# Kernel optimization log

Measured on AMD Instinct MI355X. Metric: run time of the kernel, lower is better.

## Reference

```python
import jax, jax.numpy as jnp
import numpy as np

T, H, I, E, K, L, R = 1024, 2048, 1024, 16, 2, 4, 16


def setup_inputs() -> dict:
    key = jax.random.key(0)
    ks = jax.random.split(key, 10)
    hidden_states = jax.random.normal(ks[0], (T, H), jnp.float32)
    topk_ids = jax.random.randint(ks[1], (T, K), 0, E, dtype=jnp.int32)
    topk_weights = jax.random.uniform(ks[2], (T, K), jnp.float32)
    lora_indices = jax.random.randint(ks[3], (T,), 0, L, dtype=jnp.int32)
    lora_ranks = jax.random.randint(ks[4], (L,), 1, R + 1, dtype=jnp.int32)
    scalings = jax.random.uniform(ks[5], (L,), jnp.float32) + 0.5
    w1 = jax.random.normal(ks[6], (E, 2 * I, H), jnp.float32) * 0.02  # fused gate+up
    w2 = jax.random.normal(ks[7], (E, H, I), jnp.float32) * 0.02      # down proj
    lora_a = jax.random.normal(ks[8], (L, E, R, H), jnp.float32) * 0.02
    lora_b = jax.random.normal(ks[9], (L, E, H, R), jnp.float32) * 0.02
    return dict(hidden_states=hidden_states, topk_ids=topk_ids, topk_weights=topk_weights,
                lora_indices=lora_indices, lora_ranks=lora_ranks, scalings=scalings,
                w1=w1, w2=w2, lora_a=lora_a, lora_b=lora_b)


def reference(hidden_states, topk_ids, topk_weights, lora_indices, lora_ranks, scalings,
              w1, w2, lora_a, lora_b):
    x = hidden_states  # [T, H]
    # ---- Base FusedMoE (SiLU-gated), dense over all experts then routed ----
    h1 = jnp.einsum('th,efh->tef', x, w1)                 # [T, E, 2I]
    gate, up = jnp.split(h1, 2, axis=-1)                  # [T, E, I] each
    act = jax.nn.silu(gate) * up                          # [T, E, I]
    expert_out = jnp.einsum('tei,ehi->teh', act, w2)      # [T, E, H]
    route = jnp.zeros((T, E), x.dtype).at[jnp.arange(T)[:, None], topk_ids].add(topk_weights)
    base = jnp.einsum('te,teh->th', route, expert_out)    # [T, H]
    # ---- Per-expert LoRA delta (moe_dispatch + grouped LoRA GEMM) ----
    l_pair = jnp.broadcast_to(lora_indices[:, None], (T, K)).reshape(-1)  # [P], P=T*K
    e_pair = topk_ids.reshape(-1)                                         # [P]
    valid = l_pair >= 0
    l_safe = jnp.maximum(l_pair, 0)
    flat_idx = l_safe * E + e_pair                                        # index into [L*E, ...]
    A = jnp.take(lora_a.reshape(L * E, R, H), flat_idx, axis=0)           # [P, R, H]
    B = jnp.take(lora_b.reshape(L * E, H, R), flat_idx, axis=0)           # [P, H, R]
    xp = jnp.repeat(x, K, axis=0)                                         # [P, H]
    a = jnp.einsum('ph,prh->pr', xp, A)                                   # [P, R]
    ranks = jnp.maximum(lora_ranks, 1)
    rmask = jnp.arange(R)[None, :] < ranks[l_safe][:, None]               # variable rank mask
    a = jnp.where(rmask, a, 0.0) * scalings[l_safe][:, None]
    delta = jnp.einsum('pr,phr->ph', a, B)                                # [P, H]
    delta = jnp.where(valid[:, None], delta, 0.0)
    delta = delta.reshape(T, K, H).sum(axis=1)                            # merge (token,k) pairs
    return base + delta
```

## Files before the change

kernel.cpp:

```cpp
#include <hip/hip_runtime.h>
#include <math.h>

constexpr int T = 1024;
constexpr int H = 2048;
constexpr int I = 1024;
constexpr int E = 16;
constexpr int K = 2;
constexpr int L = 4;
constexpr int R = 16;
constexpr int P = T * K;
constexpr int MT_MAX = 32;
constexpr int G_CVT = T * H / (256 * 8);
constexpr int G1 = MT_MAX * 32;
constexpr int G2 = MT_MAX * 64;

typedef __attribute__((ext_vector_type(8))) short bf16x8;
typedef __attribute__((ext_vector_type(4))) float f32x4;

__device__ inline unsigned short f2bf(float f) {
  unsigned u = __builtin_bit_cast(unsigned, f);
  u = (u + 0x7FFFu + ((u >> 16) & 1u)) >> 16;
  return (unsigned short)u;
}

__device__ inline bf16x8 pack8(f32x4 a, f32x4 b) {
  bf16x8 v;
  v[0] = (short)f2bf(a[0]); v[1] = (short)f2bf(a[1]);
  v[2] = (short)f2bf(a[2]); v[3] = (short)f2bf(a[3]);
  v[4] = (short)f2bf(b[0]); v[5] = (short)f2bf(b[1]);
  v[6] = (short)f2bf(b[2]); v[7] = (short)f2bf(b[3]);
  return v;
}

__device__ inline void st8(unsigned short* s, int r, int c, bf16x8 v) {
  int byte = ((r << 6) + c) * 2;
  byte ^= (r & 7) << 4;
  *reinterpret_cast<bf16x8*>(reinterpret_cast<char*>(s) + byte) = v;
}
__device__ inline bf16x8 ld8(const unsigned short* s, int r, int c) {
  int byte = ((r << 6) + c) * 2;
  byte ^= (r & 7) << 4;
  return *reinterpret_cast<const bf16x8*>(reinterpret_cast<const char*>(s) + byte);
}

__global__ __launch_bounds__(256) void prep_kernel(
    const float* __restrict__ x, unsigned short* __restrict__ xb,
    float* __restrict__ out,
    const int* __restrict__ topk_ids, const float* __restrict__ topk_w,
    int* __restrict__ eoff, int* __restrict__ pair_t,
    float* __restrict__ pair_w, int* __restrict__ pair_e,
    int* __restrict__ tile_e, int* __restrict__ tile_m0, int* __restrict__ ntiles) {
  const int tid = threadIdx.x;
  if (blockIdx.x < G_CVT) {
    const int i = (blockIdx.x * 256 + tid) * 8;
    f32x4 a = *reinterpret_cast<const f32x4*>(x + i);
    f32x4 b = *reinterpret_cast<const f32x4*>(x + i + 4);
    *reinterpret_cast<bf16x8*>(xb + i) = pack8(a, b);
    const f32x4 z = {0.f, 0.f, 0.f, 0.f};
    *reinterpret_cast<f32x4*>(out + i) = z;
    *reinterpret_cast<f32x4*>(out + i + 4) = z;
    return;
  }
  __shared__ int cnt[E];
  __shared__ int off[E + 1];
  __shared__ int cur[E];
  if (tid < E) cnt[tid] = 0;
  __syncthreads();
  for (int p = tid; p < P; p += 256) atomicAdd(&cnt[topk_ids[p]], 1);
  __syncthreads();
  if (tid == 0) {
    off[0] = 0;
    for (int e = 0; e < E; ++e) off[e + 1] = off[e] + cnt[e];
    int nt = 0;
    for (int e = 0; e < E; ++e)
      for (int m0 = 0; m0 < cnt[e]; m0 += 128) {
        tile_e[nt] = e;
        tile_m0[nt] = m0;
        ++nt;
      }
    *ntiles = nt;
  }
  __syncthreads();
  if (tid < E) cur[tid] = off[tid];
  if (tid <= E) eoff[tid] = off[tid];
  __syncthreads();
  for (int p = tid; p < P; p += 256) {
    const int e = topk_ids[p];
    const int pos = atomicAdd(&cur[e], 1);
    pair_t[pos] = p / K;
    pair_w[pos] = topk_w[p];
    pair_e[pos] = e;
  }
}

__global__ __launch_bounds__(256) void gemm1_lora(
    const unsigned short* __restrict__ xb, const float* __restrict__ w1,
    const int* __restrict__ eoff, const int* __restrict__ pair_t,
    const int* __restrict__ tile_e, const int* __restrict__ tile_m0,
    const int* __restrict__ ntiles, unsigned short* __restrict__ act,
    const float* __restrict__ x, const float* __restrict__ lora_a,
    const float* __restrict__ lora_b, const int* __restrict__ lora_idx,
    const int* __restrict__ lora_ranks, const float* __restrict__ scalings,
    const int* __restrict__ pair_e, float* __restrict__ out) {
  __shared__ __align__(16) char smem[24576];
  const int tid = threadIdx.x;

  if (blockIdx.x < (unsigned)G1) {
    const int bid = blockIdx.x;
    const int mt = bid >> 5;
    if (mt >= *ntiles) return;
    const int it = bid & 31;
    const int e = tile_e[mt];
    const int m0 = tile_m0[mt];
    const int beg = eoff[e];
    const int cnt = eoff[e + 1] - beg;
    const int i0 = it * 32;

    unsigned short* sX = (unsigned short*)smem;
    unsigned short* sG = (unsigned short*)(smem + 16384);
    unsigned short* sU = (unsigned short*)(smem + 20480);

    const int xr = tid >> 1, xc = (tid & 1) * 32;
    const int gr = tid >> 3, gc = (tid & 7) * 8;

    const int rm = m0 + xr;
    const int tok = (rm < cnt) ? pair_t[beg + rm] : -1;
    const unsigned short* xrow = xb + (size_t)(tok < 0 ? 0 : tok) * H + xc;
    const float* grow = w1 + ((size_t)e * (2 * I) + i0 + gr) * H + gc;
    const float* urow = grow + (size_t)I * H;

    const int lane = tid & 63, wid = tid >> 6;
    const int wm = wid << 5;
    const int fr = lane & 15, fq = lane >> 4;

    f32x4 ag[2][2], au[2][2];
#pragma unroll
    for (int a = 0; a < 2; ++a)
#pragma unroll
      for (int b = 0; b < 2; ++b) {
        ag[a][b] = {0.f, 0.f, 0.f, 0.f};
        au[a][b] = {0.f, 0.f, 0.f, 0.f};
      }

    bf16x8 rx[4];
    f32x4 rg[2], ru[2];
    const bf16x8 zero8 = {0, 0, 0, 0, 0, 0, 0, 0};

    auto LOAD = [&](int kk) {
      if (tok >= 0) {
#pragma unroll
        for (int s = 0; s < 4; ++s)
          rx[s] = *reinterpret_cast<const bf16x8*>(xrow + kk + s * 8);
      } else {
#pragma unroll
        for (int s = 0; s < 4; ++s) rx[s] = zero8;
      }
#pragma unroll
      for (int s = 0; s < 2; ++s) {
        rg[s] = *reinterpret_cast<const f32x4*>(grow + kk + s * 4);
        ru[s] = *reinterpret_cast<const f32x4*>(urow + kk + s * 4);
      }
    };

    constexpr int NT = H / 64;
    LOAD(0);
    for (int t = 0; t < NT; ++t) {
      const bf16x8 wg = pack8(rg[0], rg[1]);
      const bf16x8 wu = pack8(ru[0], ru[1]);
      __syncthreads();
      st8(sX, xr, xc + 0, rx[0]); st8(sX, xr, xc + 8, rx[1]);
      st8(sX, xr, xc + 16, rx[2]); st8(sX, xr, xc + 24, rx[3]);
      st8(sG, gr, gc, wg);
      st8(sU, gr, gc, wu);
      if (t + 1 < NT) LOAD((t + 1) * 64);
      __syncthreads();
#pragma unroll
      for (int kb = 0; kb < 2; ++kb) {
        const int k8 = (kb << 5) + (fq << 3);
        bf16x8 af[2], gf[2], uf[2];
#pragma unroll
        for (int mi = 0; mi < 2; ++mi) af[mi] = ld8(sX, wm + (mi << 4) + fr, k8);
#pragma unroll
        for (int nj = 0; nj < 2; ++nj) {
          gf[nj] = ld8(sG, (nj << 4) + fr, k8);
          uf[nj] = ld8(sU, (nj << 4) + fr, k8);
        }
#pragma unroll
        for (int mi = 0; mi < 2; ++mi)
#pragma unroll
          for (int nj = 0; nj < 2; ++nj) {
            ag[mi][nj] = __builtin_amdgcn_mfma_f32_16x16x32_bf16(af[mi], gf[nj], ag[mi][nj], 0, 0, 0);
            au[mi][nj] = __builtin_amdgcn_mfma_f32_16x16x32_bf16(af[mi], uf[nj], au[mi][nj], 0, 0, 0);
          }
      }
    }

#pragma unroll
    for (int mi = 0; mi < 2; ++mi)
#pragma unroll
      for (int q = 0; q < 4; ++q) {
        const int m = m0 + wm + (mi << 4) + (fq << 2) + q;
        if (m >= cnt) continue;
#pragma unroll
        for (int nj = 0; nj < 2; ++nj) {
          const float g = ag[mi][nj][q];
          const float u = au[mi][nj][q];
          const float s = g / (1.f + __expf(-g));
          act[(size_t)(beg + m) * I + i0 + (nj << 4) + fr] = f2bf(s * u);
        }
      }
    return;
  }

  const int p = blockIdx.x - G1;
  const int t = pair_t[p];
  const int e = pair_e[p];
  const int l = lora_idx[t];
  if (l < 0) return;
  int rank = lora_ranks[l];
  if (rank < 1) rank = 1;
  const float sc = scalings[l];

  float* a_sh = (float*)smem;
  const int wave = tid >> 6, lane = tid & 63;
  const float4* xv = reinterpret_cast<const float4*>(x + (size_t)t * H);
  const float* Ab = lora_a + (size_t)(l * E + e) * R * H;
#pragma unroll
  for (int q = 0; q < 4; ++q) {
    const int r = (wave << 2) | q;
    const float4* Av = reinterpret_cast<const float4*>(Ab + (size_t)r * H);
    float s = 0.f;
#pragma unroll
    for (int it = 0; it < H / 256; ++it) {
      const int h4 = it * 64 + lane;
      const float4 xx = xv[h4];
      const float4 aa = Av[h4];
      s += xx.x * aa.x + xx.y * aa.y + xx.z * aa.z + xx.w * aa.w;
    }
#pragma unroll
    for (int off = 32; off; off >>= 1) s += __shfl_xor(s, off);
    if (lane == 0) a_sh[r] = (r < rank) ? s * sc : 0.f;
  }
  __syncthreads();
  const float* Bb = lora_b + (size_t)(l * E + e) * H * R;
  for (int h = tid; h < H; h += 256) {
    const float4* Bv = reinterpret_cast<const float4*>(Bb + (size_t)h * R);
    float d = 0.f;
#pragma unroll
    for (int r4 = 0; r4 < 4; ++r4) {
      const float4 bb = Bv[r4];
      d += a_sh[r4 * 4 + 0] * bb.x + a_sh[r4 * 4 + 1] * bb.y +
           a_sh[r4 * 4 + 2] * bb.z + a_sh[r4 * 4 + 3] * bb.w;
    }
    atomicAdd(out + (size_t)t * H + h, d);
  }
}

__global__ __launch_bounds__(256) void gemm2_mfma(
    const unsigned short* __restrict__ act, const float* __restrict__ w2,
    const int* __restrict__ eoff, const int* __restrict__ pair_t,
    const float* __restrict__ pair_w, const int* __restrict__ tile_e,
    const int* __restrict__ tile_m0, const int* __restrict__ ntiles,
    float* __restrict__ out) {
  const int bid = blockIdx.x;
  const int mt = bid >> 6;
  if (mt >= *ntiles) return;
  const int ht = bid & 63;
  const int e = tile_e[mt];
  const int m0 = tile_m0[mt];
  const int beg = eoff[e];
  const int cnt = eoff[e + 1] - beg;
  const int h0 = ht * 32;

  __shared__ unsigned short sA[128 * 64];
  __shared__ unsigned short sB[32 * 64];

  const int tid = threadIdx.x;
  const int ar = tid >> 1, ac = (tid & 1) * 32;
  const int br = tid >> 3, bc = (tid & 7) * 8;

  const bool av = (m0 + ar) < cnt;
  const unsigned short* arow = act + (size_t)(beg + (av ? m0 + ar : 0)) * I + ac;
  const float* brow = w2 + ((size_t)e * H + h0 + br) * I + bc;

  const int lane = tid & 63, wid = tid >> 6;
  const int wm = wid << 5;
  const int fr = lane & 15, fq = lane >> 4;

  f32x4 acc[2][2];
#pragma unroll
  for (int a = 0; a < 2; ++a)
#pragma unroll
    for (int b = 0; b < 2; ++b) acc[a][b] = {0.f, 0.f, 0.f, 0.f};

  bf16x8 ra[4];
  f32x4 rb[2];

  auto LOAD = [&](int kk) {
#pragma unroll
    for (int s = 0; s < 4; ++s)
      ra[s] = *reinterpret_cast<const bf16x8*>(arow + kk + s * 8);
#pragma unroll
    for (int s = 0; s < 2; ++s)
      rb[s] = *reinterpret_cast<const f32x4*>(brow + kk + s * 4);
  };

  constexpr int NT = I / 64;
  LOAD(0);
  for (int t = 0; t < NT; ++t) {
    const bf16x8 wb = pack8(rb[0], rb[1]);
    __syncthreads();
    st8(sA, ar, ac + 0, ra[0]); st8(sA, ar, ac + 8, ra[1]);
    st8(sA, ar, ac + 16, ra[2]); st8(sA, ar, ac + 24, ra[3]);
    st8(sB, br, bc, wb);
    if (t + 1 < NT) LOAD((t + 1) * 64);
    __syncthreads();
#pragma unroll
    for (int kb = 0; kb < 2; ++kb) {
      const int k8 = (kb << 5) + (fq << 3);
      bf16x8 af[2], bf[2];
#pragma unroll
      for (int mi = 0; mi < 2; ++mi) af[mi] = ld8(sA, wm + (mi << 4) + fr, k8);
#pragma unroll
      for (int nj = 0; nj < 2; ++nj) bf[nj] = ld8(sB, (nj << 4) + fr, k8);
#pragma unroll
      for (int mi = 0; mi < 2; ++mi)
#pragma unroll
        for (int nj = 0; nj < 2; ++nj)
          acc[mi][nj] = __builtin_amdgcn_mfma_f32_16x16x32_bf16(af[mi], bf[nj], acc[mi][nj], 0, 0, 0);
    }
  }

#pragma unroll
  for (int mi = 0; mi < 2; ++mi)
#pragma unroll
    for (int q = 0; q < 4; ++q) {
      const int m = m0 + wm + (mi << 4) + (fq << 2) + q;
      if (m >= cnt) continue;
      const int tt = pair_t[beg + m];
      const float w = pair_w[beg + m];
#pragma unroll
      for (int nj = 0; nj < 2; ++nj)
        atomicAdd(out + (size_t)tt * H + h0 + (nj << 4) + fr, w * acc[mi][nj][q]);
    }
}

extern "C" void kernel_launch(void* const* d_in, const int* in_sizes, int n_in,
                              void* d_out, int out_size, void* d_ws, size_t ws_size,
                              hipStream_t stream) {
  const float* x          = (const float*)d_in[0];
  const int*   topk_ids   = (const int*)d_in[1];
  const float* topk_w     = (const float*)d_in[2];
  const int*   lora_idx   = (const int*)d_in[3];
  const int*   lora_ranks = (const int*)d_in[4];
  const float* scalings   = (const float*)d_in[5];
  const float* w1         = (const float*)d_in[6];
  const float* w2         = (const float*)d_in[7];
  const float* lora_a     = (const float*)d_in[8];
  const float* lora_b     = (const float*)d_in[9];
  float* out = (float*)d_out;

  char* ws = (char*)d_ws;
  int*   eoff    = (int*)(ws);
  int*   ntiles  = (int*)(ws + 96);
  int*   tile_e  = (int*)(ws + 256);
  int*   tile_m0 = (int*)(ws + 384);
  int*   pair_t  = (int*)(ws + 512);
  int*   pair_e  = (int*)(ws + 512 + 4 * P);
  float* pair_w  = (float*)(ws + 512 + 8 * P);
  unsigned short* xb  = (unsigned short*)(ws + 32768);
  unsigned short* act = (unsigned short*)(ws + 32768 + (size_t)T * H * 2);

  prep_kernel<<<G_CVT + 1, 256, 0, stream>>>(x, xb, out, topk_ids, topk_w, eoff,
                                             pair_t, pair_w, pair_e, tile_e, tile_m0, ntiles);
  gemm1_lora<<<G1 + P, 256, 0, stream>>>(xb, w1, eoff, pair_t, tile_e, tile_m0, ntiles,
                                         act, x, lora_a, lora_b, lora_idx, lora_ranks,
                                         scalings, pair_e, out);
  gemm2_mfma<<<G2, 256, 0, stream>>>(act, w2, eoff, pair_t, pair_w, tile_e, tile_m0,
                                     ntiles, out);
}
```

Baseline: 177.2 us.

## Merge gemm1, LoRA and gemm2 into one persistent work-queue kernel

Replaces the separate gemm1+LoRA and gemm2 launches with a single persistent kernel of 768 blocks that pulls work items from a global atomic counter. Gemm1 tiles go first, then LoRA pairs, then gemm2 tiles. Each gemm2 tile spins on a per-tile completion counter that its gemm1 tiles increment, so the two GEMM stages can overlap instead of waiting on a full kernel boundary. It also avoids launching empty blocks for nonexistent tiles. The costs are atomic queue traffic, spin-wait stalls, and a dependence on forward progress.

```diff
diff --git a/kernel.cpp b/kernel.cpp
--- a/kernel.cpp
+++ b/kernel.cpp
@@ -9,10 +9,8 @@
 constexpr int L = 4;
 constexpr int R = 16;
 constexpr int P = T * K;
-constexpr int MT_MAX = 32;
 constexpr int G_CVT = T * H / (256 * 8);
-constexpr int G1 = MT_MAX * 32;
-constexpr int G2 = MT_MAX * 64;
+constexpr int GRID = 768;
 
 typedef __attribute__((ext_vector_type(8))) short bf16x8;
 typedef __attribute__((ext_vector_type(4))) float f32x4;
@@ -49,7 +47,8 @@
     const int* __restrict__ topk_ids, const float* __restrict__ topk_w,
     int* __restrict__ eoff, int* __restrict__ pair_t,
     float* __restrict__ pair_w, int* __restrict__ pair_e,
-    int* __restrict__ tile_e, int* __restrict__ tile_m0, int* __restrict__ ntiles) {
+    int* __restrict__ tile_e, int* __restrict__ tile_m0, int* __restrict__ ntiles,
+    int* __restrict__ q, int* __restrict__ done) {
   const int tid = threadIdx.x;
   if (blockIdx.x < G_CVT) {
     const int i = (blockIdx.x * 256 + tid) * 8;
@@ -64,6 +63,8 @@
   __shared__ int cnt[E];
   __shared__ int off[E + 1];
   __shared__ int cur[E];
+  if (tid == 0) *q = 0;
+  if (tid < 32) done[tid] = 0;
   if (tid < E) cnt[tid] = 0;
   __syncthreads();
   for (int p = tid; p < P; p += 256) atomicAdd(&cnt[topk_ids[p]], 1);
@@ -93,256 +94,265 @@
   }
 }
 
-__global__ __launch_bounds__(256) void gemm1_lora(
-    const unsigned short* __restrict__ xb, const float* __restrict__ w1,
-    const int* __restrict__ eoff, const int* __restrict__ pair_t,
-    const int* __restrict__ tile_e, const int* __restrict__ tile_m0,
-    const int* __restrict__ ntiles, unsigned short* __restrict__ act,
-    const float* __restrict__ x, const float* __restrict__ lora_a,
-    const float* __restrict__ lora_b, const int* __restrict__ lora_idx,
-    const int* __restrict__ lora_ranks, const float* __restrict__ scalings,
-    const int* __restrict__ pair_e, float* __restrict__ out) {
+__global__ __launch_bounds__(256, 3) void moe_queue(
+    const unsigned short* xb, const float* w1, const float* w2,
+    const int* eoff, const int* pair_t, const float* pair_w, const int* pair_e,
+    const int* tile_e, const int* tile_m0, const int* ntiles,
+    unsigned short* act,
+    const float* x, const float* lora_a, const float* lora_b,
+    const int* lora_idx, const int* lora_ranks, const float* scalings,
+    float* out, int* q, int* done) {
   __shared__ __align__(16) char smem[24576];
+  __shared__ int sh_item;
   const int tid = threadIdx.x;
-
-  if (blockIdx.x < (unsigned)G1) {
-    const int bid = blockIdx.x;
-    const int mt = bid >> 5;
-    if (mt >= *ntiles) return;
-    const int it = bid & 31;
-    const int e = tile_e[mt];
-    const int m0 = tile_m0[mt];
-    const int beg = eoff[e];
-    const int cnt = eoff[e + 1] - beg;
-    const int i0 = it * 32;
-
-    unsigned short* sX = (unsigned short*)smem;
-    unsigned short* sG = (unsigned short*)(smem + 16384);
-    unsigned short* sU = (unsigned short*)(smem + 20480);
-
-    const int xr = tid >> 1, xc = (tid & 1) * 32;
-    const int gr = tid >> 3, gc = (tid & 7) * 8;
-
-    const int rm = m0 + xr;
-    const int tok = (rm < cnt) ? pair_t[beg + rm] : -1;
-    const unsigned short* xrow = xb + (size_t)(tok < 0 ? 0 : tok) * H + xc;
-    const float* grow = w1 + ((size_t)e * (2 * I) + i0 + gr) * H + gc;
-    const float* urow = grow + (size_t)I * H;
-
-    const int lane = tid & 63, wid = tid >> 6;
-    const int wm = wid << 5;
-    const int fr = lane & 15, fq = lane >> 4;
-
-    f32x4 ag[2][2], au[2][2];
-#pragma unroll
-    for (int a = 0; a < 2; ++a)
-#pragma unroll
-      for (int b = 0; b < 2; ++b) {
-        ag[a][b] = {0.f, 0.f, 0.f, 0.f};
-        au[a][b] = {0.f, 0.f, 0.f, 0.f};
-      }
-
-    bf16x8 rx[4];
-    f32x4 rg[2], ru[2];
-    const bf16x8 zero8 = {0, 0, 0, 0, 0, 0, 0, 0};
-
-    auto LOAD = [&](int kk) {
-      if (tok >= 0) {
+  const int nt = *ntiles;
+  const int n1 = nt * 32;
+  const int n2 = nt * 64;
+  const int total = n1 + P + n2;
+
+  for (;;) {
+    __syncthreads();
+    if (tid == 0) sh_item = atomicAdd(q, 1);
+    __syncthreads();
+    const int item = sh_item;
+    if (item >= total) break;
+
+    if (item < n1) {
+      const int mt = item >> 5;
+      const int it = item & 31;
+      const int e = tile_e[mt];
+      const int m0 = tile_m0[mt];
+      const int beg = eoff[e];
+      const int cnt = eoff[e + 1] - beg;
+      const int i0 = it * 32;
+
+      unsigned short* sX = (unsigned short*)smem;
+      unsigned short* sG = (unsigned short*)(smem + 16384);
+      unsigned short* sU = (unsigned short*)(smem + 20480);
+
+      const int xr = tid >> 1, xc = (tid & 1) * 32;
+      const int gr = tid >> 3, gc = (tid & 7) * 8;
+
+      const int rm = m0 + xr;
+      const int tok = (rm < cnt) ? pair_t[beg + rm] : -1;
+      const unsigned short* xrow = xb + (size_t)(tok < 0 ? 0 : tok) * H + xc;
+      const float* grow = w1 + ((size_t)e * (2 * I) + i0 + gr) * H + gc;
+      const float* urow = grow + (size_t)I * H;
+
+      const int lane = tid & 63, wid = tid >> 6;
+      const int wm = wid << 5;
+      const int fr = lane & 15, fq = lane >> 4;
+
+      f32x4 ag[2][2], au[2][2];
+#pragma unroll
+      for (int a = 0; a < 2; ++a)
+#pragma unroll
+        for (int b = 0; b < 2; ++b) {
+          ag[a][b] = {0.f, 0.f, 0.f, 0.f};
+          au[a][b] = {0.f, 0.f, 0.f, 0.f};
+        }
+
+      bf16x8 rx[4];
+      f32x4 rg[2], ru[2];
+      const bf16x8 zero8 = {0, 0, 0, 0, 0, 0, 0, 0};
+
+      auto LOAD = [&](int kk) {
+        if (tok >= 0) {
+#pragma unroll
+          for (int s = 0; s < 4; ++s)
+            rx[s] = *reinterpret_cast<const bf16x8*>(xrow + kk + s * 8);
+        } else {
+#pragma unroll
+          for (int s = 0; s < 4; ++s) rx[s] = zero8;
+        }
+#pragma unroll
+        for (int s = 0; s < 2; ++s) {
+          rg[s] = *reinterpret_cast<const f32x4*>(grow + kk + s * 4);
+          ru[s] = *reinterpret_cast<const f32x4*>(urow + kk + s * 4);
+        }
+      };
+
+      constexpr int NT = H / 64;
+      LOAD(0);
+      for (int t = 0; t < NT; ++t) {
+        const bf16x8 wg = pack8(rg[0], rg[1]);
+        const bf16x8 wu = pack8(ru[0], ru[1]);
+        __syncthreads();
+        st8(sX, xr, xc + 0, rx[0]); st8(sX, xr, xc + 8, rx[1]);
+        st8(sX, xr, xc + 16, rx[2]); st8(sX, xr, xc + 24, rx[3]);
+        st8(sG, gr, gc, wg);
+        st8(sU, gr, gc, wu);
+        if (t + 1 < NT) LOAD((t + 1) * 64);
+        __syncthreads();
+#pragma unroll
+        for (int kb = 0; kb < 2; ++kb) {
+          const int k8 = (kb << 5) + (fq << 3);
+          bf16x8 af[2], gf[2], uf[2];
+#pragma unroll
+          for (int mi = 0; mi < 2; ++mi) af[mi] = ld8(sX, wm + (mi << 4) + fr, k8);
+#pragma unroll
+          for (int nj = 0; nj < 2; ++nj) {
+            gf[nj] = ld8(sG, (nj << 4) + fr, k8);
+            uf[nj] = ld8(sU, (nj << 4) + fr, k8);
+          }
+#pragma unroll
+          for (int mi = 0; mi < 2; ++mi)
+#pragma unroll
+            for (int nj = 0; nj < 2; ++nj) {
+              ag[mi][nj] = __builtin_amdgcn_mfma_f32_16x16x32_bf16(af[mi], gf[nj], ag[mi][nj], 0, 0, 0);
+              au[mi][nj] = __builtin_amdgcn_mfma_f32_16x16x32_bf16(af[mi], uf[nj], au[mi][nj], 0, 0, 0);
+            }
+        }
+      }
+
+#pragma unroll
+      for (int mi = 0; mi < 2; ++mi)
+#pragma unroll
+        for (int q2 = 0; q2 < 4; ++q2) {
+          const int m = m0 + wm + (mi << 4) + (fq << 2) + q2;
+          if (m >= cnt) continue;
+#pragma unroll
+          for (int nj = 0; nj < 2; ++nj) {
+            const float g = ag[mi][nj][q2];
+            const float u = au[mi][nj][q2];
+            const float s = g / (1.f + __expf(-g));
+            act[(size_t)(beg + m) * I + i0 + (nj << 4) + fr] = f2bf(s * u);
+          }
+        }
+      __syncthreads();
+      if (tid == 0) {
+        __threadfence();
+        atomicAdd(&done[mt], 1);
+      }
+    } else if (item < n1 + P) {
+      const int p = item - n1;
+      const int t = pair_t[p];
+      const int e = pair_e[p];
+      const int l = lora_idx[t];
+      if (l >= 0) {
+        int rank = lora_ranks[l];
+        if (rank < 1) rank = 1;
+        const float sc = scalings[l];
+        float* a_sh = (float*)smem;
+        const int wave = tid >> 6, lane = tid & 63;
+        const float4* xv = reinterpret_cast<const float4*>(x + (size_t)t * H);
+        const float* Ab = lora_a + (size_t)(l * E + e) * R * H;
+#pragma unroll
+        for (int q2 = 0; q2 < 4; ++q2) {
+          const int r = (wave << 2) | q2;
+          const float4* Av = reinterpret_cast<const float4*>(Ab + (size_t)r * H);
+          float s = 0.f;
+#pragma unroll
+          for (int it2 = 0; it2 < H / 256; ++it2) {
+            const int h4 = it2 * 64 + lane;
+            const float4 xx = xv[h4];
+            const float4 aa = Av[h4];
+            s += xx.x * aa.x + xx.y * aa.y + xx.z * aa.z + xx.w * aa.w;
+          }
+#pragma unroll
+          for (int off = 32; off; off >>= 1) s += __shfl_xor(s, off);
+          if (lane == 0) a_sh[r] = (r < rank) ? s * sc : 0.f;
+        }
+        __syncthreads();
+        const float* Bb = lora_b + (size_t)(l * E + e) * H * R;
+        for (int h = tid; h < H; h += 256) {
+          const float4* Bv = reinterpret_cast<const float4*>(Bb + (size_t)h * R);
+          float d = 0.f;
+#pragma unroll
+          for (int r4 = 0; r4 < 4; ++r4) {
+            const float4 bb = Bv[r4];
+            d += a_sh[r4 * 4 + 0] * bb.x + a_sh[r4 * 4 + 1] * bb.y +
+                 a_sh[r4 * 4 + 2] * bb.z + a_sh[r4 * 4 + 3] * bb.w;
+          }
+          atomicAdd(out + (size_t)t * H + h, d);
+        }
+      }
+    } else {
+      const int g = item - n1 - P;
+      const int mt = g >> 6;
+      const int ht = g & 63;
+      while (__hip_atomic_load(&done[mt], __ATOMIC_ACQUIRE, __HIP_MEMORY_SCOPE_AGENT) < 32)
+        __builtin_amdgcn_s_sleep(8);
+      __syncthreads();
+
+      const int e = tile_e[mt];
+      const int m0 = tile_m0[mt];
+      const int beg = eoff[e];
+      const int cnt = eoff[e + 1] - beg;
+      const int h0 = ht * 32;
+
+      unsigned short* sA = (unsigned short*)smem;
+      unsigned short* sB = (unsigned short*)(smem + 16384);
+
+      const int ar = tid >> 1, ac = (tid & 1) * 32;
+      const int br = tid >> 3, bc = (tid & 7) * 8;
+
+      const bool av = (m0 + ar) < cnt;
+      const unsigned short* arow = act + (size_t)(beg + (av ? m0 + ar : 0)) * I + ac;
+      const float* brow = w2 + ((size_t)e * H + h0 + br) * I + bc;
+
+      const int lane = tid & 63, wid = tid >> 6;
+      const int wm = wid << 5;
+      const int fr = lane & 15, fq = lane >> 4;
+
+      f32x4 acc[2][2];
+#pragma unroll
+      for (int a = 0; a < 2; ++a)
+#pragma unroll
+        for (int b = 0; b < 2; ++b) acc[a][b] = {0.f, 0.f, 0.f, 0.f};
+
+      bf16x8 ra[4];
+      f32x4 rb[2];
+
+      auto LOAD = [&](int kk) {
 #pragma unroll
         for (int s = 0; s < 4; ++s)
-          rx[s] = *reinterpret_cast<const bf16x8*>(xrow + kk + s * 8);
-      } else {
-#pragma unroll
-        for (int s = 0; s < 4; ++s) rx[s] = zero8;
-      }
-#pragma unroll
-      for (int s = 0; s < 2; ++s) {
-        rg[s] = *reinterpret_cast<const f32x4*>(grow + kk + s * 4);
-        ru[s] = *reinterpret_cast<const f32x4*>(urow + kk + s * 4);
-      }
-    };
-
-    constexpr int NT = H / 64;
-    LOAD(0);
-    for (int t = 0; t < NT; ++t) {
-      const bf16x8 wg = pack8(rg[0], rg[1]);
-      const bf16x8 wu = pack8(ru[0], ru[1]);
-      __syncthreads();
-      st8(sX, xr, xc + 0, rx[0]); st8(sX, xr, xc + 8, rx[1]);
-      st8(sX, xr, xc + 16, rx[2]); st8(sX, xr, xc + 24, rx[3]);
-      st8(sG, gr, gc, wg);
-      st8(sU, gr, gc, wu);
-      if (t + 1 < NT) LOAD((t + 1) * 64);
-      __syncthreads();
-#pragma unroll
-      for (int kb = 0; kb < 2; ++kb) {
-        const int k8 = (kb << 5) + (fq << 3);
-        bf16x8 af[2], gf[2], uf[2];
-#pragma unroll
-        for (int mi = 0; mi < 2; ++mi) af[mi] = ld8(sX, wm + (mi << 4) + fr, k8);
-#pragma unroll
-        for (int nj = 0; nj < 2; ++nj) {
-          gf[nj] = ld8(sG, (nj << 4) + fr, k8);
-          uf[nj] = ld8(sU, (nj << 4) + fr, k8);
-        }
-#pragma unroll
-        for (int mi = 0; mi < 2; ++mi)
-#pragma unroll
-          for (int nj = 0; nj < 2; ++nj) {
-            ag[mi][nj] = __builtin_amdgcn_mfma_f32_16x16x32_bf16(af[mi], gf[nj], ag[mi][nj], 0, 0, 0);
-            au[mi][nj] = __builtin_amdgcn_mfma_f32_16x16x32_bf16(af[mi], uf[nj], au[mi][nj], 0, 0, 0);
-          }
-      }
-    }
-
-#pragma unroll
-    for (int mi = 0; mi < 2; ++mi)
-#pragma unroll
-      for (int q = 0; q < 4; ++q) {
-        const int m = m0 + wm + (mi << 4) + (fq << 2) + q;
-        if (m >= cnt) continue;
-#pragma unroll
-        for (int nj = 0; nj < 2; ++nj) {
-          const float g = ag[mi][nj][q];
-          const float u = au[mi][nj][q];
-          const float s = g / (1.f + __expf(-g));
-          act[(size_t)(beg + m) * I + i0 + (nj << 4) + fr] = f2bf(s * u);
-        }
-      }
-    return;
-  }
-
-  const int p = blockIdx.x - G1;
-  const int t = pair_t[p];
-  const int e = pair_e[p];
-  const int l = lora_idx[t];
-  if (l < 0) return;
-  int rank = lora_ranks[l];
-  if (rank < 1) rank = 1;
-  const float sc = scalings[l];
-
-  float* a_sh = (float*)smem;
-  const int wave = tid >> 6, lane = tid & 63;
-  const float4* xv = reinterpret_cast<const float4*>(x + (size_t)t * H);
-  const float* Ab = lora_a + (size_t)(l * E + e) * R * H;
-#pragma unroll
-  for (int q = 0; q < 4; ++q) {
-    const int r = (wave << 2) | q;
-    const float4* Av = reinterpret_cast<const float4*>(Ab + (size_t)r * H);
-    float s = 0.f;
-#pragma unroll
-    for (int it = 0; it < H / 256; ++it) {
-      const int h4 = it * 64 + lane;
-      const float4 xx = xv[h4];
-      const float4 aa = Av[h4];
-      s += xx.x * aa.x + xx.y * aa.y + xx.z * aa.z + xx.w * aa.w;
-    }
-#pragma unroll
-    for (int off = 32; off; off >>= 1) s += __shfl_xor(s, off);
-    if (lane == 0) a_sh[r] = (r < rank) ? s * sc : 0.f;
-  }
-  __syncthreads();
-  const float* Bb = lora_b + (size_t)(l * E + e) * H * R;
-  for (int h = tid; h < H; h += 256) {
-    const float4* Bv = reinterpret_cast<const float4*>(Bb + (size_t)h * R);
-    float d = 0.f;
-#pragma unroll
-    for (int r4 = 0; r4 < 4; ++r4) {
-      const float4 bb = Bv[r4];
-      d += a_sh[r4 * 4 + 0] * bb.x + a_sh[r4 * 4 + 1] * bb.y +
-           a_sh[r4 * 4 + 2] * bb.z + a_sh[r4 * 4 + 3] * bb.w;
-    }
-    atomicAdd(out + (size_t)t * H + h, d);
-  }
-}
-
-__global__ __launch_bounds__(256) void gemm2_mfma(
-    const unsigned short* __restrict__ act, const float* __restrict__ w2,
-    const int* __restrict__ eoff, const int* __restrict__ pair_t,
-    const float* __restrict__ pair_w, const int* __restrict__ tile_e,
-    const int* __restrict__ tile_m0, const int* __restrict__ ntiles,
-    float* __restrict__ out) {
-  const int bid = blockIdx.x;
-  const int mt = bid >> 6;
-  if (mt >= *ntiles) return;
-  const int ht = bid & 63;
-  const int e = tile_e[mt];
-  const int m0 = tile_m0[mt];
-  const int beg = eoff[e];
-  const int cnt = eoff[e + 1] - beg;
-  const int h0 = ht * 32;
-
-  __shared__ unsigned short sA[128 * 64];
-  __shared__ unsigned short sB[32 * 64];
-
-  const int tid = threadIdx.x;
-  const int ar = tid >> 1, ac = (tid & 1) * 32;
-  const int br = tid >> 3, bc = (tid & 7) * 8;
-
-  const bool av = (m0 + ar) < cnt;
-  const unsigned short* arow = act + (size_t)(beg + (av ? m0 + ar : 0)) * I + ac;
-  const float* brow = w2 + ((size_t)e * H + h0 + br) * I + bc;
-
-  const int lane = tid & 63, wid = tid >> 6;
-  const int wm = wid << 5;
-  const int fr = lane & 15, fq = lane >> 4;
-
-  f32x4 acc[2][2];
-#pragma unroll
-  for (int a = 0; a < 2; ++a)
-#pragma unroll
-    for (int b = 0; b < 2; ++b) acc[a][b] = {0.f, 0.f, 0.f, 0.f};
-
-  bf16x8 ra[4];
-  f32x4 rb[2];
-
-  auto LOAD = [&](int kk) {
-#pragma unroll
-    for (int s = 0; s < 4; ++s)
-      ra[s] = *reinterpret_cast<const bf16x8*>(arow + kk + s * 8);
-#pragma unroll
-    for (int s = 0; s < 2; ++s)
-      rb[s] = *reinterpret_cast<const f32x4*>(brow + kk + s * 4);
-  };
-
-  constexpr int NT = I / 64;
-  LOAD(0);
-  for (int t = 0; t < NT; ++t) {
-    const bf16x8 wb = pack8(rb[0], rb[1]);
-    __syncthreads();
-    st8(sA, ar, ac + 0, ra[0]); st8(sA, ar, ac + 8, ra[1]);
-    st8(sA, ar, ac + 16, ra[2]); st8(sA, ar, ac + 24, ra[3]);
-    st8(sB, br, bc, wb);
-    if (t + 1 < NT) LOAD((t + 1) * 64);
-    __syncthreads();
-#pragma unroll
-    for (int kb = 0; kb < 2; ++kb) {
-      const int k8 = (kb << 5) + (fq << 3);
-      bf16x8 af[2], bf[2];
-#pragma unroll
-      for (int mi = 0; mi < 2; ++mi) af[mi] = ld8(sA, wm + (mi << 4) + fr, k8);
-#pragma unroll
-      for (int nj = 0; nj < 2; ++nj) bf[nj] = ld8(sB, (nj << 4) + fr, k8);
+          ra[s] = *reinterpret_cast<const bf16x8*>(arow + kk + s * 8);
+#pragma unroll
+        for (int s = 0; s < 2; ++s)
+          rb[s] = *reinterpret_cast<const f32x4*>(brow + kk + s * 4);
+      };
+
+      constexpr int NT2 = I / 64;
+      LOAD(0);
+      for (int t = 0; t < NT2; ++t) {
+        const bf16x8 wb = pack8(rb[0], rb[1]);
+        __syncthreads();
+        st8(sA, ar, ac + 0, ra[0]); st8(sA, ar, ac + 8, ra[1]);
+        st8(sA, ar, ac + 16, ra[2]); st8(sA, ar, ac + 24, ra[3]);
+        st8(sB, br, bc, wb);
+        if (t + 1 < NT2) LOAD((t + 1) * 64);
+        __syncthreads();
+#pragma unroll
+        for (int kb = 0; kb < 2; ++kb) {
+          const int k8 = (kb << 5) + (fq << 3);
+          bf16x8 af[2], bf[2];
+#pragma unroll
+          for (int mi = 0; mi < 2; ++mi) af[mi] = ld8(sA, wm + (mi << 4) + fr, k8);
+#pragma unroll
+          for (int nj = 0; nj < 2; ++nj) bf[nj] = ld8(sB, (nj << 4) + fr, k8);
+#pragma unroll
+          for (int mi = 0; mi < 2; ++mi)
+#pragma unroll
+            for (int nj = 0; nj < 2; ++nj)
+              acc[mi][nj] = __builtin_amdgcn_mfma_f32_16x16x32_bf16(af[mi], bf[nj], acc[mi][nj], 0, 0, 0);
+        }
+      }
+
 #pragma unroll
       for (int mi = 0; mi < 2; ++mi)
 #pragma unroll
-        for (int nj = 0; nj < 2; ++nj)
-          acc[mi][nj] = __builtin_amdgcn_mfma_f32_16x16x32_bf16(af[mi], bf[nj], acc[mi][nj], 0, 0, 0);
+        for (int q2 = 0; q2 < 4; ++q2) {
+          const int m = m0 + wm + (mi << 4) + (fq << 2) + q2;
+          if (m >= cnt) continue;
+          const int tt = pair_t[beg + m];
+          const float w = pair_w[beg + m];
+#pragma unroll
+          for (int nj = 0; nj < 2; ++nj)
+            atomicAdd(out + (size_t)tt * H + h0 + (nj << 4) + fr, w * acc[mi][nj][q2]);
+        }
     }
   }
-
-#pragma unroll
-  for (int mi = 0; mi < 2; ++mi)
-#pragma unroll
-    for (int q = 0; q < 4; ++q) {
-      const int m = m0 + wm + (mi << 4) + (fq << 2) + q;
-      if (m >= cnt) continue;
-      const int tt = pair_t[beg + m];
-      const float w = pair_w[beg + m];
-#pragma unroll
-      for (int nj = 0; nj < 2; ++nj)
-        atomicAdd(out + (size_t)tt * H + h0 + (nj << 4) + fr, w * acc[mi][nj][q]);
-    }
 }
 
 extern "C" void kernel_launch(void* const* d_in, const int* in_sizes, int n_in,
@@ -363,19 +373,20 @@
   char* ws = (char*)d_ws;
   int*   eoff    = (int*)(ws);
   int*   ntiles  = (int*)(ws + 96);
-  int*   tile_e  = (int*)(ws + 256);
-  int*   tile_m0 = (int*)(ws + 384);
-  int*   pair_t  = (int*)(ws + 512);
-  int*   pair_e  = (int*)(ws + 512 + 4 * P);
-  float* pair_w  = (float*)(ws + 512 + 8 * P);
+  int*   q       = (int*)(ws + 128);
+  int*   done    = (int*)(ws + 256);
+  int*   tile_e  = (int*)(ws + 384);
+  int*   tile_m0 = (int*)(ws + 512);
+  int*   pair_t  = (int*)(ws + 1024);
+  int*   pair_e  = (int*)(ws + 1024 + 4 * P);
+  float* pair_w  = (float*)(ws + 1024 + 8 * P);
   unsigned short* xb  = (unsigned short*)(ws + 32768);
   unsigned short* act = (unsigned short*)(ws + 32768 + (size_t)T * H * 2);
 
   prep_kernel<<<G_CVT + 1, 256, 0, stream>>>(x, xb, out, topk_ids, topk_w, eoff,
-                                             pair_t, pair_w, pair_e, tile_e, tile_m0, ntiles);
-  gemm1_lora<<<G1 + P, 256, 0, stream>>>(xb, w1, eoff, pair_t, tile_e, tile_m0, ntiles,
-                                         act, x, lora_a, lora_b, lora_idx, lora_ranks,
-                                         scalings, pair_e, out);
-  gemm2_mfma<<<G2, 256, 0, stream>>>(act, w2, eoff, pair_t, pair_w, tile_e, tile_m0,
-                                     ntiles, out);
-}
+                                             pair_t, pair_w, pair_e, tile_e, tile_m0,
+                                             ntiles, q, done);
+  moe_queue<<<GRID, 256, 0, stream>>>(xb, w1, w2, eoff, pair_t, pair_w, pair_e,
+                                      tile_e, tile_m0, ntiles, act, x, lora_a, lora_b,
+                                      lora_idx, lora_ranks, scalings, out, q, done);
+}
```

After: 240.7 us. 1.36x slower.

## Halve M-tile to 64 rows and sort pairs by expert then LoRA index

Applied to the files above, without the earlier changes.

Reduces the row tile of both grouped GEMMs from 128 to 64 rows (one 16-row MFMA strip per wave), raising MT_MAX to 48 so more tiles and blocks are launched and padding waste at expert boundaries drops. The prep kernel now buckets pairs by (expert, lora) so tokens sharing a LoRA adapter are contiguous within each expert. The expert offsets stay consistent, but smaller tiles re-read the weight columns more times per expert, increasing weight traffic in exchange for better SM fill.

```diff
diff --git a/kernel.cpp b/kernel.cpp
--- a/kernel.cpp
+++ b/kernel.cpp
@@ -9,7 +9,7 @@
 constexpr int L = 4;
 constexpr int R = 16;
 constexpr int P = T * K;
-constexpr int MT_MAX = 32;
+constexpr int MT_MAX = 48;
 constexpr int G_CVT = T * H / (256 * 8);
 constexpr int G1 = MT_MAX * 32;
 constexpr int G2 = MT_MAX * 64;
@@ -47,6 +47,7 @@
     const float* __restrict__ x, unsigned short* __restrict__ xb,
     float* __restrict__ out,
     const int* __restrict__ topk_ids, const float* __restrict__ topk_w,
+    const int* __restrict__ lora_idx,
     int* __restrict__ eoff, int* __restrict__ pair_t,
     float* __restrict__ pair_w, int* __restrict__ pair_e,
     int* __restrict__ tile_e, int* __restrict__ tile_m0, int* __restrict__ ntiles) {
@@ -61,32 +62,41 @@
     *reinterpret_cast<f32x4*>(out + i + 4) = z;
     return;
   }
-  __shared__ int cnt[E];
-  __shared__ int off[E + 1];
-  __shared__ int cur[E];
-  if (tid < E) cnt[tid] = 0;
-  __syncthreads();
-  for (int p = tid; p < P; p += 256) atomicAdd(&cnt[topk_ids[p]], 1);
+  __shared__ int cnt2[E * L];
+  __shared__ int off2[E * L + 1];
+  __shared__ int cur2[E * L];
+  if (tid < E * L) cnt2[tid] = 0;
+  __syncthreads();
+  for (int p = tid; p < P; p += 256) {
+    const int e = topk_ids[p];
+    int l = lora_idx[p / K];
+    if (l < 0) l = 0;
+    atomicAdd(&cnt2[e * L + l], 1);
+  }
   __syncthreads();
   if (tid == 0) {
-    off[0] = 0;
-    for (int e = 0; e < E; ++e) off[e + 1] = off[e] + cnt[e];
+    off2[0] = 0;
+    for (int b = 0; b < E * L; ++b) off2[b + 1] = off2[b] + cnt2[b];
     int nt = 0;
-    for (int e = 0; e < E; ++e)
-      for (int m0 = 0; m0 < cnt[e]; m0 += 128) {
+    for (int e = 0; e < E; ++e) {
+      const int c = off2[(e + 1) * L] - off2[e * L];
+      for (int m0 = 0; m0 < c; m0 += 64) {
         tile_e[nt] = e;
         tile_m0[nt] = m0;
         ++nt;
       }
+    }
     *ntiles = nt;
   }
   __syncthreads();
-  if (tid < E) cur[tid] = off[tid];
-  if (tid <= E) eoff[tid] = off[tid];
+  if (tid < E * L) cur2[tid] = off2[tid];
+  if (tid <= E) eoff[tid] = off2[tid * L];
   __syncthreads();
   for (int p = tid; p < P; p += 256) {
     const int e = topk_ids[p];
-    const int pos = atomicAdd(&cur[e], 1);
+    int l = lora_idx[p / K];
+    if (l < 0) l = 0;
+    const int pos = atomicAdd(&cur2[e * L + l], 1);
     pair_t[pos] = p / K;
     pair_w[pos] = topk_w[p];
     pair_e[pos] = e;
@@ -102,7 +112,7 @@
     const float* __restrict__ lora_b, const int* __restrict__ lora_idx,
     const int* __restrict__ lora_ranks, const float* __restrict__ scalings,
     const int* __restrict__ pair_e, float* __restrict__ out) {
-  __shared__ __align__(16) char smem[24576];
+  __shared__ __align__(16) char smem[16384];
   const int tid = threadIdx.x;
 
   if (blockIdx.x < (unsigned)G1) {
@@ -117,10 +127,10 @@
     const int i0 = it * 32;
 
     unsigned short* sX = (unsigned short*)smem;
-    unsigned short* sG = (unsigned short*)(smem + 16384);
-    unsigned short* sU = (unsigned short*)(smem + 20480);
-
-    const int xr = tid >> 1, xc = (tid & 1) * 32;
+    unsigned short* sG = (unsigned short*)(smem + 8192);
+    unsigned short* sU = (unsigned short*)(smem + 12288);
+
+    const int xr = tid >> 2, xc = (tid & 3) * 16;
     const int gr = tid >> 3, gc = (tid & 7) * 8;
 
     const int rm = m0 + xr;
@@ -130,36 +140,31 @@
     const float* urow = grow + (size_t)I * H;
 
     const int lane = tid & 63, wid = tid >> 6;
-    const int wm = wid << 5;
+    const int wm = wid << 4;
     const int fr = lane & 15, fq = lane >> 4;
 
-    f32x4 ag[2][2], au[2][2];
-#pragma unroll
-    for (int a = 0; a < 2; ++a)
-#pragma unroll
-      for (int b = 0; b < 2; ++b) {
-        ag[a][b] = {0.f, 0.f, 0.f, 0.f};
-        au[a][b] = {0.f, 0.f, 0.f, 0.f};
-      }
-
-    bf16x8 rx[4];
+    f32x4 ag[2], au[2];
+#pragma unroll
+    for (int b = 0; b < 2; ++b) {
+      ag[b] = {0.f, 0.f, 0.f, 0.f};
+      au[b] = {0.f, 0.f, 0.f, 0.f};
+    }
+
+    bf16x8 rx[2];
     f32x4 rg[2], ru[2];
     const bf16x8 zero8 = {0, 0, 0, 0, 0, 0, 0, 0};
 
     auto LOAD = [&](int kk) {
       if (tok >= 0) {
-#pragma unroll
-        for (int s = 0; s < 4; ++s)
-          rx[s] = *reinterpret_cast<const bf16x8*>(xrow + kk + s * 8);
+        rx[0] = *reinterpret_cast<const bf16x8*>(xrow + kk);
+        rx[1] = *reinterpret_cast<const bf16x8*>(xrow + kk + 8);
       } else {
-#pragma unroll
-        for (int s = 0; s < 4; ++s) rx[s] = zero8;
+        rx[0] = zero8; rx[1] = zero8;
       }
-#pragma unroll
-      for (int s = 0; s < 2; ++s) {
-        rg[s] = *reinterpret_cast<const f32x4*>(grow + kk + s * 4);
-        ru[s] = *reinterpret_cast<const f32x4*>(urow + kk + s * 4);
-      }
+      rg[0] = *reinterpret_cast<const f32x4*>(grow + kk);
+      rg[1] = *reinterpret_cast<const f32x4*>(grow + kk + 4);
+      ru[0] = *reinterpret_cast<const f32x4*>(urow + kk);
+      ru[1] = *reinterpret_cast<const f32x4*>(urow + kk + 4);
     };
 
     constexpr int NT = H / 64;
@@ -168,8 +173,7 @@
       const bf16x8 wg = pack8(rg[0], rg[1]);
       const bf16x8 wu = pack8(ru[0], ru[1]);
       __syncthreads();
-      st8(sX, xr, xc + 0, rx[0]); st8(sX, xr, xc + 8, rx[1]);
-      st8(sX, xr, xc + 16, rx[2]); st8(sX, xr, xc + 24, rx[3]);
+      st8(sX, xr, xc, rx[0]); st8(sX, xr, xc + 8, rx[1]);
       st8(sG, gr, gc, wg);
       st8(sU, gr, gc, wu);
       if (t + 1 < NT) LOAD((t + 1) * 64);
@@ -177,38 +181,33 @@
 #pragma unroll
       for (int kb = 0; kb < 2; ++kb) {
         const int k8 = (kb << 5) + (fq << 3);
-        bf16x8 af[2], gf[2], uf[2];
-#pragma unroll
-        for (int mi = 0; mi < 2; ++mi) af[mi] = ld8(sX, wm + (mi << 4) + fr, k8);
+        bf16x8 af = ld8(sX, wm + fr, k8);
+        bf16x8 gf[2], uf[2];
 #pragma unroll
         for (int nj = 0; nj < 2; ++nj) {
           gf[nj] = ld8(sG, (nj << 4) + fr, k8);
           uf[nj] = ld8(sU, (nj << 4) + fr, k8);
         }
 #pragma unroll
-        for (int mi = 0; mi < 2; ++mi)
-#pragma unroll
-          for (int nj = 0; nj < 2; ++nj) {
-            ag[mi][nj] = __builtin_amdgcn_mfma_f32_16x16x32_bf16(af[mi], gf[nj], ag[mi][nj], 0, 0, 0);
-            au[mi][nj] = __builtin_amdgcn_mfma_f32_16x16x32_bf16(af[mi], uf[nj], au[mi][nj], 0, 0, 0);
-          }
-      }
-    }
-
-#pragma unroll
-    for (int mi = 0; mi < 2; ++mi)
-#pragma unroll
-      for (int q = 0; q < 4; ++q) {
-        const int m = m0 + wm + (mi << 4) + (fq << 2) + q;
-        if (m >= cnt) continue;
-#pragma unroll
         for (int nj = 0; nj < 2; ++nj) {
-          const float g = ag[mi][nj][q];
-          const float u = au[mi][nj][q];
-          const float s = g / (1.f + __expf(-g));
-          act[(size_t)(beg + m) * I + i0 + (nj << 4) + fr] = f2bf(s * u);
+          ag[nj] = __builtin_amdgcn_mfma_f32_16x16x32_bf16(af, gf[nj], ag[nj], 0, 0, 0);
+          au[nj] = __builtin_amdgcn_mfma_f32_16x16x32_bf16(af, uf[nj], au[nj], 0, 0, 0);
         }
       }
+    }
+
+#pragma unroll
+    for (int q = 0; q < 4; ++q) {
+      const int m = m0 + wm + (fq << 2) + q;
+      if (m >= cnt) continue;
+#pragma unroll
+      for (int nj = 0; nj < 2; ++nj) {
+        const float g = ag[nj][q];
+        const float u = au[nj][q];
+        const float s = g / (1.f + __expf(-g));
+        act[(size_t)(beg + m) * I + i0 + (nj << 4) + fr] = f2bf(s * u);
+      }
+    }
     return;
   }
 
@@ -231,8 +230,8 @@
     const float4* Av = reinterpret_cast<const float4*>(Ab + (size_t)r * H);
     float s = 0.f;
 #pragma unroll
-    for (int it = 0; it < H / 256; ++it) {
-      const int h4 = it * 64 + lane;
+    for (int it2 = 0; it2 < H / 256; ++it2) {
+      const int h4 = it2 * 64 + lane;
       const float4 xx = xv[h4];
       const float4 aa = Av[h4];
       s += xx.x * aa.x + xx.y * aa.y + xx.z * aa.z + xx.w * aa.w;
@@ -272,11 +271,11 @@
   const int cnt = eoff[e + 1] - beg;
   const int h0 = ht * 32;
 
-  __shared__ unsigned short sA[128 * 64];
+  __shared__ unsigned short sA[64 * 64];
   __shared__ unsigned short sB[32 * 64];
 
   const int tid = threadIdx.x;
-  const int ar = tid >> 1, ac = (tid & 1) * 32;
+  const int ar = tid >> 2, ac = (tid & 3) * 16;
   const int br = tid >> 3, bc = (tid & 7) * 8;
 
   const bool av = (m0 + ar) < cnt;
@@ -284,65 +283,55 @@
   const float* brow = w2 + ((size_t)e * H + h0 + br) * I + bc;
 
   const int lane = tid & 63, wid = tid >> 6;
-  const int wm = wid << 5;
+  const int wm = wid << 4;
   const int fr = lane & 15, fq = lane >> 4;
 
-  f32x4 acc[2][2];
-#pragma unroll
-  for (int a = 0; a < 2; ++a)
-#pragma unroll
-    for (int b = 0; b < 2; ++b) acc[a][b] = {0.f, 0.f, 0.f, 0.f};
-
-  bf16x8 ra[4];
+  f32x4 acc[2];
+#pragma unroll
+  for (int b = 0; b < 2; ++b) acc[b] = {0.f, 0.f, 0.f, 0.f};
+
+  bf16x8 ra[2];
   f32x4 rb[2];
 
   auto LOAD = [&](int kk) {
-#pragma unroll
-    for (int s = 0; s < 4; ++s)
-      ra[s] = *reinterpret_cast<const bf16x8*>(arow + kk + s * 8);
-#pragma unroll
-    for (int s = 0; s < 2; ++s)
-      rb[s] = *reinterpret_cast<const f32x4*>(brow + kk + s * 4);
+    ra[0] = *reinterpret_cast<const bf16x8*>(arow + kk);
+    ra[1] = *reinterpret_cast<const bf16x8*>(arow + kk + 8);
+    rb[0] = *reinterpret_cast<const f32x4*>(brow + kk);
+    rb[1] = *reinterpret_cast<const f32x4*>(brow + kk + 4);
   };
 
-  constexpr int NT = I / 64;
+  constexpr int NT2 = I / 64;
   LOAD(0);
-  for (int t = 0; t < NT; ++t) {
+  for (int t = 0; t < NT2; ++t) {
     const bf16x8 wb = pack8(rb[0], rb[1]);
     __syncthreads();
-    st8(sA, ar, ac + 0, ra[0]); st8(sA, ar, ac + 8, ra[1]);
-    st8(sA, ar, ac + 16, ra[2]); st8(sA, ar, ac + 24, ra[3]);
+    st8(sA, ar, ac, ra[0]); st8(sA, ar, ac + 8, ra[1]);
     st8(sB, br, bc, wb);
-    if (t + 1 < NT) LOAD((t + 1) * 64);
+    if (t + 1 < NT2) LOAD((t + 1) * 64);
     __syncthreads();
 #pragma unroll
     for (int kb = 0; kb < 2; ++kb) {
       const int k8 = (kb << 5) + (fq << 3);
-      bf16x8 af[2], bf[2];
-#pragma unroll
-      for (int mi = 0; mi < 2; ++mi) af[mi] = ld8(sA, wm + (mi << 4) + fr, k8);
+      bf16x8 af = ld8(sA, wm + fr, k8);
+      bf16x8 bf[2];
 #pragma unroll
       for (int nj = 0; nj < 2; ++nj) bf[nj] = ld8(sB, (nj << 4) + fr, k8);
 #pragma unroll
-      for (int mi = 0; mi < 2; ++mi)
-#pragma unroll
-        for (int nj = 0; nj < 2; ++nj)
-          acc[mi][nj] = __builtin_amdgcn_mfma_f32_16x16x32_bf16(af[mi], bf[nj], acc[mi][nj], 0, 0, 0);
-    }
-  }
-
-#pragma unroll
-  for (int mi = 0; mi < 2; ++mi)
-#pragma unroll
-    for (int q = 0; q < 4; ++q) {
-      const int m = m0 + wm + (mi << 4) + (fq << 2) + q;
-      if (m >= cnt) continue;
-      const int tt = pair_t[beg + m];
-      const float w = pair_w[beg + m];
-#pragma unroll
       for (int nj = 0; nj < 2; ++nj)
-        atomicAdd(out + (size_t)tt * H + h0 + (nj << 4) + fr, w * acc[mi][nj][q]);
-    }
+        acc[nj] = __builtin_amdgcn_mfma_f32_16x16x32_bf16(af, bf[nj], acc[nj], 0, 0, 0);
+    }
+  }
+
+#pragma unroll
+  for (int q = 0; q < 4; ++q) {
+    const int m = m0 + wm + (fq << 2) + q;
+    if (m >= cnt) continue;
+    const int tt = pair_t[beg + m];
+    const float w = pair_w[beg + m];
+#pragma unroll
+    for (int nj = 0; nj < 2; ++nj)
+      atomicAdd(out + (size_t)tt * H + h0 + (nj << 4) + fr, w * acc[nj][q]);
+  }
 }
 
 extern "C" void kernel_launch(void* const* d_in, const int* in_sizes, int n_in,
@@ -364,15 +353,16 @@
   int*   eoff    = (int*)(ws);
   int*   ntiles  = (int*)(ws + 96);
   int*   tile_e  = (int*)(ws + 256);
-  int*   tile_m0 = (int*)(ws + 384);
-  int*   pair_t  = (int*)(ws + 512);
-  int*   pair_e  = (int*)(ws + 512 + 4 * P);
-  float* pair_w  = (float*)(ws + 512 + 8 * P);
+  int*   tile_m0 = (int*)(ws + 512);
+  int*   pair_t  = (int*)(ws + 1024);
+  int*   pair_e  = (int*)(ws + 1024 + 4 * P);
+  float* pair_w  = (float*)(ws + 1024 + 8 * P);
   unsigned short* xb  = (unsigned short*)(ws + 32768);
   unsigned short* act = (unsigned short*)(ws + 32768 + (size_t)T * H * 2);
 
-  prep_kernel<<<G_CVT + 1, 256, 0, stream>>>(x, xb, out, topk_ids, topk_w, eoff,
-                                             pair_t, pair_w, pair_e, tile_e, tile_m0, ntiles);
+  prep_kernel<<<G_CVT + 1, 256, 0, stream>>>(x, xb, out, topk_ids, topk_w, lora_idx,
+                                             eoff, pair_t, pair_w, pair_e, tile_e,
+                                             tile_m0, ntiles);
   gemm1_lora<<<G1 + P, 256, 0, stream>>>(xb, w1, eoff, pair_t, tile_e, tile_m0, ntiles,
                                          act, x, lora_a, lora_b, lora_idx, lora_ranks,
                                          scalings, pair_e, out);
```

Result: slower. 187.2 us (+5.6%).
